# Kernel optimization log

Hardware: AMD Instinct MI355X
Metric: run time of the kernel (lower is better)

Reference implementation:

```python
import jax, jax.numpy as jnp
import numpy as np
import math

N_RES, N_EDGE = 10000, 320000
C_S, C_Z, C_H, H, PQ, PV = 384, 128, 16, 12, 4, 8
INF, EPS = 1e5, 1e-8


def _lin(key, din, dout):
    k1, k2 = jax.random.split(key)
    w = jax.random.normal(k1, (din, dout), jnp.float32) * (1.0 / np.sqrt(din))
    b = jax.random.normal(k2, (dout,), jnp.float32) * 0.02
    return w, b


def setup_inputs() -> dict:
    key = jax.random.key(0)
    ks = jax.random.split(key, 16)
    s = jax.random.normal(ks[0], (N_RES, C_S), jnp.float32)
    z = jax.random.normal(ks[1], (N_EDGE, C_Z), jnp.float32)
    edge_index = jax.random.randint(ks[2], (2, N_EDGE), 0, N_RES, jnp.int32)
    rot = jnp.linalg.qr(jax.random.normal(ks[3], (N_RES, 3, 3), jnp.float32))[0]
    trans = jax.random.normal(ks[4], (N_RES, 3), jnp.float32)
    mask = jnp.ones((N_RES,), jnp.float32)
    wq, bq = _lin(ks[5], C_S, H * C_H)
    wkv, bkv = _lin(ks[6], C_S, 2 * H * C_H)
    wqp, bqp = _lin(ks[7], C_S, H * PQ * 3)
    wkvp, bkvp = _lin(ks[8], C_S, H * (PQ + PV) * 3)
    wb, bb = _lin(ks[9], C_Z, H)
    wdz, bdz = _lin(ks[10], C_Z, C_Z // 4)
    head_w = jax.random.normal(ks[11], (H,), jnp.float32) * 0.1
    wout, bout = _lin(ks[12], H * (C_Z // 4 + C_H + PV * 4), C_S)
    return dict(s=s, z=z, rot=rot, trans=trans, mask=mask, edge_index=edge_index,
                wq=wq, bq=bq, wkv=wkv, bkv=bkv, wqp=wqp, bqp=bqp, wkvp=wkvp, bkvp=bkvp,
                wb=wb, bb=bb, wdz=wdz, bdz=bdz, head_w=head_w, wout=wout, bout=bout)


def reference(s, z, rot, trans, mask, edge_index, wq, bq, wkv, bkv, wqp, bqp,
              wkvp, bkvp, wb, bb, wdz, bdz, head_w, wout, bout):
    n = s.shape[0]
    src, dst = edge_index[0], edge_index[1]  # key-side, query-side

    q = (s @ wq + bq).reshape(n, H, C_H)
    kv = (s @ wkv + bkv).reshape(n, H, 2 * C_H)
    k, v = kv[..., :C_H], kv[..., C_H:]

    def make_pts(x, p):
        # torch: split [n, H*p*3] into 3 chunks of H*p, stack on last dim -> [n, H*p, 3]
        x = jnp.stack(jnp.split(x, 3, axis=-1), axis=-1)
        x = jnp.einsum('nij,npj->npi', rot, x) + trans[:, None, :]  # global frame
        return x.reshape(n, H, p, 3)

    q_pts = make_pts(s @ wqp + bqp, PQ)                 # [n, H, PQ, 3]
    kv_pts = make_pts(s @ wkvp + bkvp, PQ + PV)
    k_pts, v_pts = kv_pts[..., :PQ, :], kv_pts[..., PQ:, :]

    b = z @ wb + bb                                      # [E, H]
    a = jnp.einsum('ehc,ehc->eh', q[dst], k[src]) * math.sqrt(1.0 / (3 * C_H))
    a = a + math.sqrt(1.0 / 3) * b

    disp = q_pts[dst] - k_pts[src]                       # [E, H, PQ, 3]
    hw = jax.nn.softplus(head_w) * math.sqrt(1.0 / (3 * (PQ * 9.0 / 2)))
    pt_att = -0.5 * jnp.einsum('ehp,h->eh', jnp.sum(disp * disp, axis=-1), hw)

    edge_mask = INF * (mask[src] * mask[dst] - 1.0)
    a = a + pt_att + edge_mask[:, None]

    # segment softmax over edges grouped by destination node
    m = jax.lax.stop_gradient(jax.ops.segment_max(a, dst, num_segments=n))
    ea = jnp.exp(a - m[dst])
    a = ea / (jax.ops.segment_sum(ea, dst, num_segments=n)[dst] + 1e-16)

    o = jax.ops.segment_sum(a[..., None] * v[src], dst, num_segments=n).reshape(n, -1)

    o_pt = jax.ops.segment_sum(a[..., None, None] * v_pts[src], dst, num_segments=n)  # [n,H,PV,3]
    o_pt = jnp.einsum('nji,nhpj->nhpi', rot, o_pt - trans[:, None, None, :])  # invert_apply
    o_pt_norm = jnp.sqrt(jnp.sum(o_pt * o_pt, axis=-1) + EPS).reshape(n, -1)
    o_pt = o_pt.reshape(n, H * PV, 3)

    pair_z = z @ wdz + bdz                               # [E, c_z//4]
    o_pair = jax.ops.segment_sum(a[..., None] * pair_z[:, None, :], dst,
                                 num_segments=n).reshape(n, -1)

    feats = jnp.concatenate([o, o_pt[..., 0], o_pt[..., 1], o_pt[..., 2],
                             o_pt_norm, o_pair], axis=-1)
    return feats @ wout + bout
```

## Files before the change

kernel.cpp:

```cpp
#include <hip/hip_runtime.h>
#include <hip/hip_bf16.h>
#include <math.h>

#define N_RESC 10000
#define N_EDGEC 320000
#define C_SC 384
#define C_ZC 128
#define AGG_D 864
#define FEAT_D 960
#define OUT_D 384

#define S1C 0.14433756729740643f
#define S2C 0.5773502691896258f
#define SHWC 0.13608276348795434f

__global__ void k_zero(int* cursor) {
    int i = blockIdx.x * 256 + threadIdx.x;
    if (i < N_RESC) cursor[i] = 0;
}

__global__ void k_hist(const int* __restrict__ ei, int* cursor) {
    int e = blockIdx.x * 256 + threadIdx.x;
    if (e < N_EDGEC) atomicAdd(&cursor[ei[N_EDGEC + e]], 1);
}

__global__ __launch_bounds__(1024) void k_scan(int* cursor, int* rowptr) {
    __shared__ int buf[1024];
    __shared__ int carry_s;
    int t = threadIdx.x;
    if (t == 0) carry_s = 0;
    __syncthreads();
    for (int ch = 0; ch < 10; ++ch) {
        int idx = ch * 1024 + t;
        int v = (idx < N_RESC) ? cursor[idx] : 0;
        buf[t] = v;
        __syncthreads();
        for (int off = 1; off < 1024; off <<= 1) {
            int x = (t >= off) ? buf[t - off] : 0;
            __syncthreads();
            buf[t] += x;
            __syncthreads();
        }
        int incl = buf[t];
        int excl = incl - v;
        int base = carry_s;
        int total = buf[1023];
        if (idx < N_RESC) { rowptr[idx] = base + excl; cursor[idx] = base + excl; }
        __syncthreads();
        if (t == 0) carry_s = base + total;
        __syncthreads();
    }
    if (t == 0) rowptr[N_RESC] = carry_s;
}

__global__ void k_scatter(const int* __restrict__ ei, int* cursor, int* csr, int* src_csr) {
    int e = blockIdx.x * 256 + threadIdx.x;
    if (e < N_EDGEC) {
        int d = ei[N_EDGEC + e];
        int s = ei[e];
        int pos = atomicAdd(&cursor[d], 1);
        csr[pos] = e;
        src_csr[pos] = s;
    }
}

__global__ __launch_bounds__(256) void k_wpack(
    const float* __restrict__ wq, const float* __restrict__ bq,
    const float* __restrict__ wkv, const float* __restrict__ bkv,
    const float* __restrict__ wqp, const float* __restrict__ bqp,
    const float* __restrict__ wkvp, const float* __restrict__ bkvp,
    float* __restrict__ wpack, float* __restrict__ bpack) {
    int idx = blockIdx.x * 256 + threadIdx.x;
    if (idx < 384 * 1152) {
        int j = idx / 1152, c = idx % 1152;
        float v;
        if (c < 192)      v = wq[j * 192 + c];
        else if (c < 576) v = wkv[j * 384 + (c - 192)];
        else if (c < 720) v = wqp[j * 144 + (c - 576)];
        else              v = wkvp[j * 432 + (c - 720)];
        wpack[idx] = v;
    }
    if (idx < 1152) {
        float b;
        if (idx < 192)      b = bq[idx];
        else if (idx < 576) b = bkv[idx - 192];
        else if (idx < 720) b = bqp[idx - 576];
        else                b = bkvp[idx - 720];
        bpack[idx] = b;
    }
}

#define BM 64
#define BN 128
#define BK 32
__global__ __launch_bounds__(256) void k_proj(const float* __restrict__ s,
    const float* __restrict__ wpack, const float* __restrict__ bpack,
    float* __restrict__ qh, float* __restrict__ kh, float* __restrict__ vh,
    float* __restrict__ praw) {
    __shared__ float sT[BK][BM + 4];
    __shared__ float wt[BK][BN];
    int t = threadIdx.x;
    int bm0 = blockIdx.x * BM;
    int bn0 = blockIdx.y * BN;
    int tcol = t & 31;
    int trow = t >> 5;
    int c0 = tcol * 4;
    int r0 = trow * 8;

    int srow = t >> 2;
    int skoff = (t & 3) * 8;
    int gsrow = min(bm0 + srow, N_RESC - 1);
    const float* srcp = s + (long)gsrow * C_SC + skoff;

    float acc[8][4];
    #pragma unroll
    for (int i = 0; i < 8; i++)
        #pragma unroll
        for (int j = 0; j < 4; j++) acc[i][j] = 0.f;

    for (int k0 = 0; k0 < C_SC; k0 += BK) {
        float4 sa = *(const float4*)(srcp + k0);
        float4 sb = *(const float4*)(srcp + k0 + 4);
        sT[skoff + 0][srow] = sa.x; sT[skoff + 1][srow] = sa.y;
        sT[skoff + 2][srow] = sa.z; sT[skoff + 3][srow] = sa.w;
        sT[skoff + 4][srow] = sb.x; sT[skoff + 5][srow] = sb.y;
        sT[skoff + 6][srow] = sb.z; sT[skoff + 7][srow] = sb.w;
        #pragma unroll
        for (int q = 0; q < 4; q++) {
            int kk = (t >> 5) + q * 8;
            *(float4*)&wt[kk][c0] =
                *(const float4*)(wpack + (long)(k0 + kk) * 1152 + bn0 + c0);
        }
        __syncthreads();
        #pragma unroll
        for (int k = 0; k < BK; k++) {
            float4 a0 = *(const float4*)&sT[k][r0];
            float4 a1 = *(const float4*)&sT[k][r0 + 4];
            float4 b  = *(const float4*)&wt[k][c0];
            float av0 = a0.x, av1 = a0.y, av2 = a0.z, av3 = a0.w;
            float av4 = a1.x, av5 = a1.y, av6 = a1.z, av7 = a1.w;
            acc[0][0] = fmaf(av0, b.x, acc[0][0]); acc[0][1] = fmaf(av0, b.y, acc[0][1]);
            acc[0][2] = fmaf(av0, b.z, acc[0][2]); acc[0][3] = fmaf(av0, b.w, acc[0][3]);
            acc[1][0] = fmaf(av1, b.x, acc[1][0]); acc[1][1] = fmaf(av1, b.y, acc[1][1]);
            acc[1][2] = fmaf(av1, b.z, acc[1][2]); acc[1][3] = fmaf(av1, b.w, acc[1][3]);
            acc[2][0] = fmaf(av2, b.x, acc[2][0]); acc[2][1] = fmaf(av2, b.y, acc[2][1]);
            acc[2][2] = fmaf(av2, b.z, acc[2][2]); acc[2][3] = fmaf(av2, b.w, acc[2][3]);
            acc[3][0] = fmaf(av3, b.x, acc[3][0]); acc[3][1] = fmaf(av3, b.y, acc[3][1]);
            acc[3][2] = fmaf(av3, b.z, acc[3][2]); acc[3][3] = fmaf(av3, b.w, acc[3][3]);
            acc[4][0] = fmaf(av4, b.x, acc[4][0]); acc[4][1] = fmaf(av4, b.y, acc[4][1]);
            acc[4][2] = fmaf(av4, b.z, acc[4][2]); acc[4][3] = fmaf(av4, b.w, acc[4][3]);
            acc[5][0] = fmaf(av5, b.x, acc[5][0]); acc[5][1] = fmaf(av5, b.y, acc[5][1]);
            acc[5][2] = fmaf(av5, b.z, acc[5][2]); acc[5][3] = fmaf(av5, b.w, acc[5][3]);
            acc[6][0] = fmaf(av6, b.x, acc[6][0]); acc[6][1] = fmaf(av6, b.y, acc[6][1]);
            acc[6][2] = fmaf(av6, b.z, acc[6][2]); acc[6][3] = fmaf(av6, b.w, acc[6][3]);
            acc[7][0] = fmaf(av7, b.x, acc[7][0]); acc[7][1] = fmaf(av7, b.y, acc[7][1]);
            acc[7][2] = fmaf(av7, b.z, acc[7][2]); acc[7][3] = fmaf(av7, b.w, acc[7][3]);
        }
        __syncthreads();
    }
    #pragma unroll
    for (int j = 0; j < 4; j++) {
        int c = bn0 + c0 + j;
        float bv = bpack[c];
        #pragma unroll
        for (int i = 0; i < 8; i++) {
            int n = bm0 + r0 + i;
            if (n < N_RESC) {
                float val = acc[i][j] + bv;
                if (c < 192) qh[(long)n * 192 + c] = val;
                else if (c < 576) {
                    int cc = c - 192; int h = cc >> 5, r = cc & 31;
                    if (r < 16) kh[(long)n * 192 + h * 16 + r] = val;
                    else        vh[(long)n * 192 + h * 16 + (r - 16)] = val;
                } else praw[(long)n * 576 + (c - 576)] = val;
            }
        }
    }
}

__global__ __launch_bounds__(192) void k_rot(const float* __restrict__ praw,
    const float* __restrict__ rot, const float* __restrict__ trans,
    float* __restrict__ qpts, float* __restrict__ kpts, float* __restrict__ vpts) {
    int n = blockIdx.x;
    int t = threadIdx.x;
    __shared__ float R[9], T[3];
    if (t < 9) R[t] = rot[n * 9 + t];
    if (t < 3) T[t] = trans[n * 3 + t];
    __syncthreads();
    const float* pr = praw + (long)n * 576;
    if (t < 48) {
        float x0 = pr[t], x1 = pr[48 + t], x2 = pr[96 + t];
        #pragma unroll
        for (int i = 0; i < 3; i++)
            qpts[(long)n * 144 + t * 3 + i] = R[i*3+0]*x0 + R[i*3+1]*x1 + R[i*3+2]*x2 + T[i];
    } else {
        int p = t - 48;
        float x0 = pr[144 + p], x1 = pr[288 + p], x2 = pr[432 + p];
        int h = p / 12, pp = p % 12;
        #pragma unroll
        for (int i = 0; i < 3; i++) {
            float val = R[i*3+0]*x0 + R[i*3+1]*x1 + R[i*3+2]*x2 + T[i];
            if (pp < 4) kpts[(long)n * 144 + (h * 4 + pp) * 3 + i] = val;
            else        vpts[(long)n * 288 + (h * 8 + (pp - 4)) * 3 + i] = val;
        }
    }
}

__global__ __launch_bounds__(256) void k_zproj(const float* __restrict__ z,
    const int* __restrict__ csr,
    const float* __restrict__ wb, const float* __restrict__ bb,
    const float* __restrict__ wdz, const float* __restrict__ bdz,
    float* __restrict__ b_e, float* __restrict__ pairz) {
    int t = threadIdx.x;
    long pos = (long)blockIdx.x * 256 + t;
    long e = csr[pos];
    float acc[44];
    #pragma unroll
    for (int c = 0; c < 12; c++) acc[c] = bb[c];
    #pragma unroll
    for (int c = 0; c < 32; c++) acc[12 + c] = bdz[c];
    const float4* zrow = reinterpret_cast<const float4*>(z + e * C_ZC);
    for (int j4 = 0; j4 < 32; j4++) {
        float4 zv = zrow[j4];
        #pragma unroll
        for (int u = 0; u < 4; u++) {
            float zs = (u == 0) ? zv.x : (u == 1) ? zv.y : (u == 2) ? zv.z : zv.w;
            int j = j4 * 4 + u;
            #pragma unroll
            for (int c = 0; c < 12; c++) acc[c] = fmaf(zs, wb[j * 12 + c], acc[c]);
            #pragma unroll
            for (int c = 0; c < 32; c++) acc[12 + c] = fmaf(zs, wdz[j * 32 + c], acc[12 + c]);
        }
    }
    float4* bo = reinterpret_cast<float4*>(b_e + pos * 12);
    #pragma unroll
    for (int q = 0; q < 3; q++)
        bo[q] = make_float4(acc[q*4], acc[q*4+1], acc[q*4+2], acc[q*4+3]);
    float4* po = reinterpret_cast<float4*>(pairz + pos * 32);
    #pragma unroll
    for (int q = 0; q < 8; q++)
        po[q] = make_float4(acc[12+q*4], acc[12+q*4+1], acc[12+q*4+2], acc[12+q*4+3]);
}

#define CAPL 256
__global__ __launch_bounds__(256) void k_logit(const int* __restrict__ rowptr,
    const int* __restrict__ src_csr,
    const float* __restrict__ qh, const float* __restrict__ kh,
    const float* __restrict__ qpts, const float* __restrict__ kpts,
    const float* __restrict__ mask, const float* __restrict__ head_w,
    const float* __restrict__ b_e, float* __restrict__ alog) {
    int n = blockIdx.x;
    int t = threadIdx.x;
    __shared__ float qf[192], qp[144], hws[12];
    __shared__ int slist[CAPL];
    if (t < 192) qf[t] = qh[(long)n * 192 + t];
    if (t < 144) qp[t] = qpts[(long)n * 144 + t];
    if (t < 12)  hws[t] = log1pf(expf(head_w[t])) * SHWC;
    float mdst = mask[n];
    int row0 = rowptr[n];
    int deg = rowptr[n + 1] - row0;
    int w = t >> 6, l = t & 63, c = l & 15, hq = l >> 4;
    for (int cs = 0; cs < deg; cs += CAPL) {
        int cnt = min(CAPL, deg - cs);
        __syncthreads();
        for (int i = t; i < cnt; i += 256) slist[i] = src_csr[row0 + cs + i];
        __syncthreads();
        for (int i = w * 2; i < cnt; i += 8) {
            int i1 = min(i + 1, cnt - 1);
            int s0 = slist[i], s1 = slist[i1];
            int pos0 = row0 + cs + i, pos1 = row0 + cs + i1;
            float em0 = 100000.0f * (mask[s0] * mdst - 1.0f);
            float em1 = 100000.0f * (mask[s1] * mdst - 1.0f);
            float kv0[3], kv1[3];
            #pragma unroll
            for (int tp = 0; tp < 3; tp++) {
                kv0[tp] = kh[(long)s0 * 192 + tp * 64 + l];
                kv1[tp] = kh[(long)s1 * 192 + tp * 64 + l];
            }
            float kp0[3] = {0.f,0.f,0.f}, kp1[3] = {0.f,0.f,0.f};
            if (c < 12) {
                #pragma unroll
                for (int tp = 0; tp < 3; tp++) {
                    int h = tp * 4 + hq;
                    kp0[tp] = kpts[(long)s0 * 144 + h * 12 + c];
                    kp1[tp] = kpts[(long)s1 * 144 + h * 12 + c];
                }
            }
            float be0[3] = {0.f,0.f,0.f}, be1[3] = {0.f,0.f,0.f};
            if (c == 0) {
                #pragma unroll
                for (int tp = 0; tp < 3; tp++) {
                    int h = tp * 4 + hq;
                    be0[tp] = b_e[(long)pos0 * 12 + h];
                    be1[tp] = b_e[(long)pos1 * 12 + h];
                }
            }
            #pragma unroll
            for (int tp = 0; tp < 3; tp++) {
                int h = tp * 4 + hq;
                float qfv = S1C * qf[h * 16 + c];
                float val0 = qfv * kv0[tp];
                float val1 = qfv * kv1[tp];
                if (c < 12) {
                    float qpv = qp[h * 12 + c];
                    float hw = -0.5f * hws[h];
                    float d0 = qpv - kp0[tp];
                    float d1 = qpv - kp1[tp];
                    val0 = fmaf(hw * d0, d0, val0);
                    val1 = fmaf(hw * d1, d1, val1);
                }
                val0 += __shfl_xor(val0, 8, 16); val1 += __shfl_xor(val1, 8, 16);
                val0 += __shfl_xor(val0, 4, 16); val1 += __shfl_xor(val1, 4, 16);
                val0 += __shfl_xor(val0, 2, 16); val1 += __shfl_xor(val1, 2, 16);
                val0 += __shfl_xor(val0, 1, 16); val1 += __shfl_xor(val1, 1, 16);
                if (c == 0) {
                    alog[(long)pos0 * 12 + h] = val0 + S2C * be0[tp] + em0;
                    if (i1 != i)
                        alog[(long)pos1 * 12 + h] = val1 + S2C * be1[tp] + em1;
                }
            }
        }
    }
}

#define CAPE 256
__global__ __launch_bounds__(256) void k_agg(const int* __restrict__ rowptr,
    const int* __restrict__ src_csr,
    const float* __restrict__ alog, const float* __restrict__ vh,
    const float* __restrict__ vpts, const float* __restrict__ pairz,
    float* __restrict__ agg) {
    int n = blockIdx.x;
    int t = threadIdx.x;
    __shared__ float red[16 * 12];
    __shared__ float mh[12], linv[12];
    __shared__ float al[CAPE * 12];
    __shared__ int sl_[CAPE];
    int row0 = rowptr[n];
    int deg = rowptr[n + 1] - row0;
    int g = t >> 4, l16 = t & 15;
    if (l16 < 12) {
        float lm = -1e30f;
        for (int i = g; i < deg; i += 16)
            lm = fmaxf(lm, alog[(long)(row0 + i) * 12 + l16]);
        red[g * 12 + l16] = lm;
    }
    __syncthreads();
    if (t < 12) {
        float m = -1e30f;
        for (int gg = 0; gg < 16; gg++) m = fmaxf(m, red[gg * 12 + t]);
        mh[t] = m;
    }
    __syncthreads();
    if (l16 < 12) {
        float m = mh[l16];
        float ls = 0.f;
        for (int i = g; i < deg; i += 16)
            ls += expf(alog[(long)(row0 + i) * 12 + l16] - m);
        red[g * 12 + l16] = ls;
    }
    __syncthreads();
    if (t < 12) {
        float ssum = 0.f;
        for (int gg = 0; gg < 16; gg++) ssum += red[gg * 12 + t];
        linv[t] = 1.f / (ssum + 1e-16f);
    }

    const float* base = nullptr;
    int scale = 0, hk = 0, use_e = 0;
    int comp = t * 4;
    if (comp < 192)      { base = vh + comp; scale = 192; hk = comp >> 4; }
    else if (comp < 480) { int idx = comp - 192; base = vpts + idx; scale = 288; hk = idx / 24; }
    else if (comp < 864) { int idx = comp - 480; base = pairz + (idx & 31); scale = 32; hk = idx >> 5; use_e = 1; }
    float4 acc = make_float4(0.f, 0.f, 0.f, 0.f);

    for (int cs = 0; cs < deg; cs += CAPE) {
        int cnt = min(CAPE, deg - cs);
        int p0 = row0 + cs;
        __syncthreads();
        for (int i = t; i < cnt * 12; i += 256) {
            int h = i % 12;
            al[i] = expf(alog[(long)p0 * 12 + i] - mh[h]) * linv[h];
        }
        for (int i = t; i < cnt; i += 256) sl_[i] = src_csr[p0 + i];
        __syncthreads();
        if (t < 216) {
            int i = 0;
            for (; i + 4 <= cnt; i += 4) {
                int i0 = use_e ? (p0 + i)     : sl_[i];
                int i1 = use_e ? (p0 + i + 1) : sl_[i+1];
                int i2 = use_e ? (p0 + i + 2) : sl_[i+2];
                int i3 = use_e ? (p0 + i + 3) : sl_[i+3];
                float4 v0 = *(const float4*)(base + (long)i0 * scale);
                float4 v1 = *(const float4*)(base + (long)i1 * scale);
                float4 v2 = *(const float4*)(base + (long)i2 * scale);
                float4 v3 = *(const float4*)(base + (long)i3 * scale);
                float w0 = al[i * 12 + hk];
                float w1 = al[(i+1) * 12 + hk];
                float w2 = al[(i+2) * 12 + hk];
                float w3 = al[(i+3) * 12 + hk];
                acc.x = fmaf(w0, v0.x, acc.x); acc.y = fmaf(w0, v0.y, acc.y);
                acc.z = fmaf(w0, v0.z, acc.z); acc.w = fmaf(w0, v0.w, acc.w);
                acc.x = fmaf(w1, v1.x, acc.x); acc.y = fmaf(w1, v1.y, acc.y);
                acc.z = fmaf(w1, v1.z, acc.z); acc.w = fmaf(w1, v1.w, acc.w);
                acc.x = fmaf(w2, v2.x, acc.x); acc.y = fmaf(w2, v2.y, acc.y);
                acc.z = fmaf(w2, v2.z, acc.z); acc.w = fmaf(w2, v2.w, acc.w);
                acc.x = fmaf(w3, v3.x, acc.x); acc.y = fmaf(w3, v3.y, acc.y);
                acc.z = fmaf(w3, v3.z, acc.z); acc.w = fmaf(w3, v3.w, acc.w);
            }
            for (; i < cnt; i++) {
                int ii = use_e ? (p0 + i) : sl_[i];
                float4 v = *(const float4*)(base + (long)ii * scale);
                float w = al[i * 12 + hk];
                acc.x = fmaf(w, v.x, acc.x); acc.y = fmaf(w, v.y, acc.y);
                acc.z = fmaf(w, v.z, acc.z); acc.w = fmaf(w, v.w, acc.w);
            }
        }
    }
    if (t < 216) *(float4*)(agg + (long)n * AGG_D + comp) = acc;
}

#define NT_F 8
__global__ __launch_bounds__(192) void k_final(const float* __restrict__ agg,
    const float* __restrict__ rot, const float* __restrict__ trans,
    const float* __restrict__ wout, const float* __restrict__ bout,
    float* __restrict__ out) {
    __shared__ float f[NT_F][FEAT_D];
    int t = threadIdx.x;
    int node0 = blockIdx.x * NT_F;
    for (int idx = t; idx < NT_F * 192; idx += 192) {
        int nt = idx / 192, c = idx % 192;
        f[nt][c] = agg[(long)(node0 + nt) * AGG_D + c];
    }
    for (int idx = t; idx < NT_F * 96; idx += 192) {
        int nt = idx / 96, p = idx % 96;
        int n = node0 + nt;
        const float* a = agg + (long)n * AGG_D;
        float gx = a[192 + p * 3 + 0] - trans[n * 3 + 0];
        float gy = a[192 + p * 3 + 1] - trans[n * 3 + 1];
        float gz = a[192 + p * 3 + 2] - trans[n * 3 + 2];
        const float* R = rot + (long)n * 9;
        float lx = R[0] * gx + R[3] * gy + R[6] * gz;
        float ly = R[1] * gx + R[4] * gy + R[7] * gz;
        float lz = R[2] * gx + R[5] * gy + R[8] * gz;
        f[nt][192 + p] = lx;
        f[nt][288 + p] = ly;
        f[nt][384 + p] = lz;
        f[nt][480 + p] = sqrtf(lx * lx + ly * ly + lz * lz + 1e-8f);
    }
    for (int idx = t; idx < NT_F * 384; idx += 192) {
        int nt = idx / 384, q = idx % 384;
        f[nt][576 + q] = agg[(long)(node0 + nt) * AGG_D + 480 + q];
    }
    __syncthreads();
    float acc0[NT_F], acc1[NT_F];
    float b0 = bout[t], b1 = bout[t + 192];
    #pragma unroll
    for (int nt = 0; nt < NT_F; nt++) { acc0[nt] = b0; acc1[nt] = b1; }
    for (int j = 0; j < FEAT_D; j += 4) {
        float4 fv[NT_F];
        #pragma unroll
        for (int nt = 0; nt < NT_F; nt++) fv[nt] = *(const float4*)&f[nt][j];
        #pragma unroll
        for (int u = 0; u < 4; u++) {
            float w0 = wout[(j + u) * OUT_D + t];
            float w1 = wout[(j + u) * OUT_D + t + 192];
            #pragma unroll
            for (int nt = 0; nt < NT_F; nt++) {
                float fvu = (u == 0) ? fv[nt].x : (u == 1) ? fv[nt].y : (u == 2) ? fv[nt].z : fv[nt].w;
                acc0[nt] = fmaf(fvu, w0, acc0[nt]);
                acc1[nt] = fmaf(fvu, w1, acc1[nt]);
            }
        }
    }
    #pragma unroll
    for (int nt = 0; nt < NT_F; nt++) {
        out[(long)(node0 + nt) * OUT_D + t] = acc0[nt];
        out[(long)(node0 + nt) * OUT_D + t + 192] = acc1[nt];
    }
}

extern "C" void kernel_launch(void* const* d_in, const int* in_sizes, int n_in,
                              void* d_out, int out_size, void* d_ws, size_t ws_size,
                              hipStream_t stream) {
    const float* s     = (const float*)d_in[0];
    const float* z     = (const float*)d_in[1];
    const float* rot   = (const float*)d_in[2];
    const float* trans = (const float*)d_in[3];
    const float* mask  = (const float*)d_in[4];
    const int*   ei    = (const int*)d_in[5];
    const float* wq    = (const float*)d_in[6];
    const float* bq    = (const float*)d_in[7];
    const float* wkv   = (const float*)d_in[8];
    const float* bkv   = (const float*)d_in[9];
    const float* wqp   = (const float*)d_in[10];
    const float* bqp   = (const float*)d_in[11];
    const float* wkvp  = (const float*)d_in[12];
    const float* bkvp  = (const float*)d_in[13];
    const float* wb    = (const float*)d_in[14];
    const float* bb    = (const float*)d_in[15];
    const float* wdz   = (const float*)d_in[16];
    const float* bdz   = (const float*)d_in[17];
    const float* head_w= (const float*)d_in[18];
    const float* wout  = (const float*)d_in[19];
    const float* bout  = (const float*)d_in[20];
    float* out = (float*)d_out;

    float* ws    = (float*)d_ws;
    float* qh    = ws;
    float* kh    = qh + 1920000;
    float* vh    = kh + 1920000;
    float* qpts  = vh + 1920000;
    float* kpts  = qpts + 1440000;
    float* vpts  = kpts + 1440000;
    float* b_e   = vpts + 2880000;
    float* pairz = b_e + 3840000;
    float* alog  = pairz + 10240000;
    float* agg   = alog + 3840000;
    float* praw  = agg;
    float* wpack = agg + 5760000;
    float* bpack = wpack + 442368;
    int* rowptr  = (int*)(agg + 8640000);
    int* cursor  = rowptr + 10004;
    int* csr     = cursor + 10000;
    int* src_csr = csr + N_EDGEC;

    k_zero<<<(N_RESC + 255) / 256, 256, 0, stream>>>(cursor);
    k_hist<<<(N_EDGEC + 255) / 256, 256, 0, stream>>>(ei, cursor);
    k_scan<<<1, 1024, 0, stream>>>(cursor, rowptr);
    k_scatter<<<(N_EDGEC + 255) / 256, 256, 0, stream>>>(ei, cursor, csr, src_csr);

    k_wpack<<<(384 * 1152 + 255) / 256, 256, 0, stream>>>(wq, bq, wkv, bkv, wqp, bqp,
                                                          wkvp, bkvp, wpack, bpack);
    dim3 pgrid((N_RESC + BM - 1) / BM, 1152 / BN);
    k_proj<<<pgrid, 256, 0, stream>>>(s, wpack, bpack, qh, kh, vh, praw);
    k_rot<<<N_RESC, 192, 0, stream>>>(praw, rot, trans, qpts, kpts, vpts);

    k_zproj<<<N_EDGEC / 256, 256, 0, stream>>>(z, csr, wb, bb, wdz, bdz, b_e, pairz);

    k_logit<<<N_RESC, 256, 0, stream>>>(rowptr, src_csr, qh, kh, qpts, kpts,
                                        mask, head_w, b_e, alog);

    k_agg<<<N_RESC, 256, 0, stream>>>(rowptr, src_csr, alog, vh, vpts, pairz, agg);

    k_final<<<N_RESC / NT_F, 192, 0, stream>>>(agg, rot, trans, wout, bout, out);
}
```

Baseline: 895.7 us.

## Read z rows in edge order via LDS staging and scatter outputs by CSR position

k_zproj now iterates edges in their original order rather than CSR order. Each block cooperatively loads its 256 z rows in coalesced float4 chunks into padded shared memory, then each thread reads its own row from LDS. Outputs are written to the CSR slot through a new epos array filled in k_scatter. This replaces the random, per-thread strided global reads of 512-byte z rows with contiguous block loads, at the cost of scattered output writes, an extra index array, and block barriers.

Result: slower. 916.3 us (+2.3%).

```diff
diff --git a/kernel.cpp b/kernel.cpp
--- a/kernel.cpp
+++ b/kernel.cpp
@@ -53,7 +53,8 @@
     if (t == 0) rowptr[N_RESC] = carry_s;
 }
 
-__global__ void k_scatter(const int* __restrict__ ei, int* cursor, int* csr, int* src_csr) {
+__global__ void k_scatter(const int* __restrict__ ei, int* cursor, int* csr,
+                          int* src_csr, int* epos) {
     int e = blockIdx.x * 256 + threadIdx.x;
     if (e < N_EDGEC) {
         int d = ei[N_EDGEC + e];
@@ -61,6 +62,7 @@
         int pos = atomicAdd(&cursor[d], 1);
         csr[pos] = e;
         src_csr[pos] = s;
+        epos[e] = pos;
     }
 }
 
@@ -207,31 +209,44 @@
 }
 
 __global__ __launch_bounds__(256) void k_zproj(const float* __restrict__ z,
-    const int* __restrict__ csr,
+    const int* __restrict__ epos,
     const float* __restrict__ wb, const float* __restrict__ bb,
     const float* __restrict__ wdz, const float* __restrict__ bdz,
     float* __restrict__ b_e, float* __restrict__ pairz) {
-    int t = threadIdx.x;
-    long pos = (long)blockIdx.x * 256 + t;
-    long e = csr[pos];
+    __shared__ float zl[256][33];
+    int t = threadIdx.x;
+    long e0 = (long)blockIdx.x * 256;
+    const float* zbase = z + e0 * C_ZC;
     float acc[44];
     #pragma unroll
     for (int c = 0; c < 12; c++) acc[c] = bb[c];
     #pragma unroll
     for (int c = 0; c < 32; c++) acc[12 + c] = bdz[c];
-    const float4* zrow = reinterpret_cast<const float4*>(z + e * C_ZC);
-    for (int j4 = 0; j4 < 32; j4++) {
-        float4 zv = zrow[j4];
-        #pragma unroll
-        for (int u = 0; u < 4; u++) {
-            float zs = (u == 0) ? zv.x : (u == 1) ? zv.y : (u == 2) ? zv.z : zv.w;
-            int j = j4 * 4 + u;
+
+    for (int ch = 0; ch < 4; ch++) {
+        __syncthreads();
+        #pragma unroll
+        for (int k = 0; k < 8; k++) {
+            int idx4 = t + k * 256;
+            int row = idx4 >> 3, j4 = idx4 & 7;
+            float4 v = *(const float4*)(zbase + (long)row * C_ZC + ch * 32 + j4 * 4);
+            zl[row][j4 * 4 + 0] = v.x;
+            zl[row][j4 * 4 + 1] = v.y;
+            zl[row][j4 * 4 + 2] = v.z;
+            zl[row][j4 * 4 + 3] = v.w;
+        }
+        __syncthreads();
+        #pragma unroll
+        for (int j = 0; j < 32; j++) {
+            float zs = zl[t][j];
+            int jg = ch * 32 + j;
             #pragma unroll
-            for (int c = 0; c < 12; c++) acc[c] = fmaf(zs, wb[j * 12 + c], acc[c]);
+            for (int c = 0; c < 12; c++) acc[c] = fmaf(zs, wb[jg * 12 + c], acc[c]);
             #pragma unroll
-            for (int c = 0; c < 32; c++) acc[12 + c] = fmaf(zs, wdz[j * 32 + c], acc[12 + c]);
-        }
-    }
+            for (int c = 0; c < 32; c++) acc[12 + c] = fmaf(zs, wdz[jg * 32 + c], acc[12 + c]);
+        }
+    }
+    long pos = epos[e0 + t];
     float4* bo = reinterpret_cast<float4*>(b_e + pos * 12);
     #pragma unroll
     for (int q = 0; q < 3; q++)
@@ -523,11 +538,12 @@
     int* cursor  = rowptr + 10004;
     int* csr     = cursor + 10000;
     int* src_csr = csr + N_EDGEC;
+    int* epos    = src_csr + N_EDGEC;
 
     k_zero<<<(N_RESC + 255) / 256, 256, 0, stream>>>(cursor);
     k_hist<<<(N_EDGEC + 255) / 256, 256, 0, stream>>>(ei, cursor);
     k_scan<<<1, 1024, 0, stream>>>(cursor, rowptr);
-    k_scatter<<<(N_EDGEC + 255) / 256, 256, 0, stream>>>(ei, cursor, csr, src_csr);
+    k_scatter<<<(N_EDGEC + 255) / 256, 256, 0, stream>>>(ei, cursor, csr, src_csr, epos);
 
     k_wpack<<<(384 * 1152 + 255) / 256, 256, 0, stream>>>(wq, bq, wkv, bkv, wqp, bqp,
                                                           wkvp, bkvp, wpack, bpack);
@@ -535,7 +551,7 @@
     k_proj<<<pgrid, 256, 0, stream>>>(s, wpack, bpack, qh, kh, vh, praw);
     k_rot<<<N_RESC, 192, 0, stream>>>(praw, rot, trans, qpts, kpts, vpts);
 
-    k_zproj<<<N_EDGEC / 256, 256, 0, stream>>>(z, csr, wb, bb, wdz, bdz, b_e, pairz);
+    k_zproj<<<N_EDGEC / 256, 256, 0, stream>>>(z, epos, wb, bb, wdz, bdz, b_e, pairz);
 
     k_logit<<<N_RESC, 256, 0, stream>>>(rowptr, src_csr, qh, kh, qpts, kpts,
                                         mask, head_w, b_e, alog);
```
